# Kernel tuning notes

Hardware: AMD Instinct MI355X
Metric: run time of the kernel (lower is better)

The kernel has to match this reference:

```python
import jax, jax.numpy as jnp
import numpy as np

DIM = 768
NUM_HEADS = 12
HEAD_DIM = DIM // NUM_HEADS


def setup_inputs() -> dict:
    key = jax.random.key(0)
    k1, k2, k3 = jax.random.split(key, 3)
    B, N, C = 8, 4096, DIM
    x = jax.random.normal(k1, (B, N, C), dtype=jnp.float32)
    # torch nn.Linear weights are (out_features, in_features)
    W_qkv = jax.random.normal(k2, (3 * C, C), dtype=jnp.float32) * 0.02
    b_qkv = jnp.zeros((3 * C,), dtype=jnp.float32)
    W_proj = jax.random.normal(k3, (C, C), dtype=jnp.float32) * 0.02
    b_proj = jnp.zeros((C,), dtype=jnp.float32)
    return {"x": x, "W_qkv": W_qkv, "b_qkv": b_qkv, "W_proj": W_proj, "b_proj": b_proj}


def reference(x, W_qkv, b_qkv, W_proj, b_proj):
    B, N, C = x.shape
    H, D = NUM_HEADS, HEAD_DIM
    # qkv projection -> (3, B, H, N, D)
    qkv = (x @ W_qkv.T + b_qkv).reshape(B, N, 3, H, D).transpose(2, 0, 3, 1, 4)
    q, k, v = qkv[0], qkv[1], qkv[2]
    # feature map: elu(x) + 1 (positive kernel features)
    q = jax.nn.elu(q) + 1.0
    k = jax.nn.elu(k) + 1.0
    # kernelized linear attention: (K^T V) then Q (K^T V)
    kv = jnp.einsum('bhnd,bhnv->bhdv', k, v)          # (B,H,D,D)
    out = jnp.einsum('bhnd,bhdv->bhnv', q, kv)        # (B,H,N,D)
    k_sum = k.sum(axis=2)                             # (B,H,D)
    normalizer = jnp.einsum('bhnd,bhd->bhn', q, k_sum) + 1e-06
    out = out / normalizer[..., None]
    out = out.transpose(0, 2, 1, 3).reshape(B, N, C)
    out = out @ W_proj.T + b_proj
    return out
```

## Files before the change

kernel.cpp:

```cpp
#include <hip/hip_runtime.h>
#include <hip/hip_fp16.h>
#include <math.h>

#define NHEADS 12
#define SEQ 4096
#define BATCH 8

typedef _Float16 half8 __attribute__((ext_vector_type(8)));
typedef float floatx4 __attribute__((ext_vector_type(4)));

__global__ void zero_kernel(float* p, int n) {
  int i = blockIdx.x * 256 + threadIdx.x;
  if (i < n) p[i] = 0.f;
}

__global__ void cast_f2h(const float* __restrict__ in, __half* __restrict__ out, int n) {
  int i = (blockIdx.x * 256 + threadIdx.x) * 4;
  if (i < n) {
    float4 v = *(const float4*)&in[i];
    ushort4 o;
    o.x = __half_as_ushort(__float2half(v.x));
    o.y = __half_as_ushort(__float2half(v.y));
    o.z = __half_as_ushort(__float2half(v.z));
    o.w = __half_as_ushort(__float2half(v.w));
    *(ushort4*)&out[i] = o;
  }
}

__device__ __forceinline__ void stage_tile(const __half* __restrict__ gbase, int ldg,
                                           _Float16* lds, int t) {
#pragma unroll
  for (int it = 0; it < 2; ++it) {
    const int s  = it * 256 + t;
    const int mp = s >> 3, ps = s & 7;
    const int p  = ps ^ (mp & 7);
    const int r  = mp * 2 + (p >> 2);
    const int q  = p & 3;
    const __half* g = gbase + (size_t)r * ldg + q * 8;
    _Float16* dst = lds + (s >> 6) * 512;
    __builtin_amdgcn_global_load_lds((const __attribute__((address_space(1))) void*)g,
                                     (__attribute__((address_space(3))) void*)dst, 16, 0, 0);
  }
}
__device__ __forceinline__ half8 read_frag(const _Float16* lds, int row, int quad) {
  const int mp = row >> 1;
  const int p  = ((row & 1) << 2) | quad;
  const int ps = p ^ (mp & 7);
  return *(const half8*)(lds + (mp * 8 + ps) * 8);
}

__device__ __forceinline__ void write_l64(_Float16* lds, int row, int col, float v) {
  lds[row * 64 + ((((col >> 3) ^ (row & 7))) << 3) + (col & 7)] = (_Float16)v;
}
__device__ __forceinline__ half8 read_l64c(const _Float16* lds, int row, int c) {
  return *(const half8*)(lds + row * 64 + ((c ^ (row & 7)) << 3));
}

template<int MODE>
__global__ __launch_bounds__(256) void hgemm_kernel(
    const __half* __restrict__ A, const __half* __restrict__ W,
    const float* __restrict__ bias,
    __half* __restrict__ outK, __half* __restrict__ outV,
    float* __restrict__ outF, int colBase)
{
  const int K = 768;
  __shared__ __align__(16) _Float16 sh[16384];
  _Float16* As = sh;
  _Float16* Bs = sh + 4096;
  const int t    = threadIdx.x;
  const int w    = t >> 6;
  const int l    = t & 63;
  const int quad = l >> 4;
  const int mrow = l & 15;
  const int m0   = blockIdx.x * 128;
  const int j0   = blockIdx.y * 128;
  const int wr   = (w >> 1) * 64;
  const int wc   = (w & 1) * 64;

  floatx4 acc[4][4];
#pragma unroll
  for (int i = 0; i < 4; ++i)
#pragma unroll
    for (int j = 0; j < 4; ++j) acc[i][j] = (floatx4){0.f, 0.f, 0.f, 0.f};

  for (int k0 = 0; k0 < K; k0 += 32) {
    __syncthreads();
    stage_tile(A + (size_t)m0 * K + k0, K, As, t);
    stage_tile(W + (size_t)(colBase + j0) * K + k0, K, Bs, t);
    __syncthreads();
    half8 af[4], bf[4];
#pragma unroll
    for (int i = 0; i < 4; ++i) af[i] = read_frag(As, wr + i * 16 + mrow, quad);
#pragma unroll
    for (int j = 0; j < 4; ++j) bf[j] = read_frag(Bs, wc + j * 16 + mrow, quad);
#pragma unroll
    for (int i = 0; i < 4; ++i)
#pragma unroll
      for (int j = 0; j < 4; ++j)
        acc[i][j] = __builtin_amdgcn_mfma_f32_16x16x32_f16(af[i], bf[j], acc[i][j], 0, 0, 0);
  }

  if (MODE == 0) {
#pragma unroll
    for (int j = 0; j < 4; ++j) {
      const int col = colBase + j0 + wc + j * 16 + mrow;
      const float bsv = bias[col];
#pragma unroll
      for (int i = 0; i < 4; ++i)
#pragma unroll
        for (int r = 0; r < 4; ++r) {
          const int m = m0 + wr + i * 16 + quad * 4 + r;
          outF[(size_t)m * 768 + col] = acc[i][j][r] + bsv;
        }
    }
    return;
  }

  const int col0 = colBase + j0 + wc;
  const int t3   = col0 / 768;
  const int h    = (col0 - t3 * 768) >> 6;
  __half* dst    = (t3 == 1) ? outK : outV;
  const int m0w  = m0 + wr;
  const int b_   = m0w >> 12;
  const int n0w  = m0w & 4095;
  _Float16* scr  = sh + w * 4096;

  __syncthreads();
#pragma unroll
  for (int j = 0; j < 4; ++j) {
    const int col = j * 16 + mrow;
    const float bsv = bias[col0 + col];
#pragma unroll
    for (int i = 0; i < 4; ++i)
#pragma unroll
      for (int r = 0; r < 4; ++r) {
        const int row = i * 16 + quad * 4 + r;
        float val = acc[i][j][r] + bsv;
        if (t3 == 1) val = (val > 0.f) ? (val + 1.f) : expf(val);
        write_l64(scr, row, col, val);
      }
  }
  __syncthreads();
  const size_t gb = ((size_t)(b_ * NHEADS + h) * SEQ + n0w) * 64;
#pragma unroll
  for (int it = 0; it < 8; ++it) {
    const int row = it * 8 + (l >> 3);
    const int c   = l & 7;
    half8 vv = read_l64c(scr, row, c);
    *(half8*)((_Float16*)dst + gb + (size_t)row * 64 + c * 8) = vv;
  }
}

__global__ __launch_bounds__(256) void kv_kernel(
    const __half* __restrict__ k, const __half* __restrict__ v,
    float* __restrict__ kv, float* __restrict__ ksum)
{
  __shared__ float ks[32 * 64];
  __shared__ float vs[32 * 64];
  const int bh = blockIdx.x;
  const int s  = blockIdx.y;
  const int t  = threadIdx.x;
  const int w  = t >> 6;
  const int l  = t & 63;
  const size_t base = (size_t)bh * SEQ * 64 + (size_t)s * 512 * 64;

  float acc[16];
#pragma unroll
  for (int i = 0; i < 16; ++i) acc[i] = 0.f;
  float kspart = 0.f;

  const int nn0 = t >> 3;
  const int c8  = (t & 7) * 8;

  for (int chunk = 0; chunk < 512; chunk += 32) {
    __syncthreads();
    {
      half8 kk = *(const half8*)&k[base + (size_t)(chunk + nn0) * 64 + c8];
      half8 vv = *(const half8*)&v[base + (size_t)(chunk + nn0) * 64 + c8];
#pragma unroll
      for (int e = 0; e < 8; ++e) {
        ks[nn0 * 64 + c8 + e] = (float)kk[e];
        vs[nn0 * 64 + c8 + e] = (float)vv[e];
      }
    }
    __syncthreads();
#pragma unroll 4
    for (int nn = 0; nn < 32; ++nn) {
      const float ve = vs[nn * 64 + l];
      const float4* kr = (const float4*)&ks[nn * 64 + w * 16];
      float4 k0 = kr[0], k1 = kr[1], k2 = kr[2], k3 = kr[3];
      acc[0]  += k0.x * ve; acc[1]  += k0.y * ve; acc[2]  += k0.z * ve; acc[3]  += k0.w * ve;
      acc[4]  += k1.x * ve; acc[5]  += k1.y * ve; acc[6]  += k1.z * ve; acc[7]  += k1.w * ve;
      acc[8]  += k2.x * ve; acc[9]  += k2.y * ve; acc[10] += k2.z * ve; acc[11] += k2.w * ve;
      acc[12] += k3.x * ve; acc[13] += k3.y * ve; acc[14] += k3.z * ve; acc[15] += k3.w * ve;
      kspart += ks[nn * 64 + l];
    }
  }
#pragma unroll
  for (int i = 0; i < 16; ++i) {
    const int d = w * 16 + i;
    atomicAdd(&kv[((size_t)bh * 64 + d) * 64 + l], acc[i]);
  }
  if (t < 64) atomicAdd(&ksum[(size_t)bh * 64 + l], kspart);
}

__global__ __launch_bounds__(256) void qattn_kernel(
    const __half* __restrict__ A, const __half* __restrict__ W,
    const float* __restrict__ bias,
    const float* __restrict__ kvg, const float* __restrict__ ksumg,
    __half* __restrict__ att)
{
  const int K = 768;
  __shared__ __align__(16) _Float16 sh[24576];
  _Float16* As = sh;
  _Float16* Bs = sh + 4096;
  __shared__ float norms[256];
  __shared__ float ksums[128];
  const int t    = threadIdx.x;
  const int w    = t >> 6;
  const int l    = t & 63;
  const int quad = l >> 4;
  const int mrow = l & 15;
  const int m0   = blockIdx.x * 128;
  const int j0   = blockIdx.y * 128;
  const int wr   = (w >> 1) * 64;
  const int wc   = (w & 1) * 64;
  const int b_   = m0 >> 12;
  const int h0   = j0 >> 6;

  {
    _Float16* kvT0 = sh + 16384;
#pragma unroll
    for (int ii = 0; ii < 32; ++ii) {
      const int gidx = ii * 256 + t;
      const int head = gidx >> 12;
      const int r    = gidx & 4095;
      const float val = kvg[(size_t)(b_ * NHEADS + h0 + head) * 4096 + r];
      write_l64(kvT0 + head * 4096, r & 63, r >> 6, val);
    }
    if (t < 128) ksums[t] = ksumg[(size_t)(b_ * NHEADS + h0 + (t >> 6)) * 64 + (t & 63)];
  }

  floatx4 acc[4][4];
#pragma unroll
  for (int i = 0; i < 4; ++i)
#pragma unroll
    for (int j = 0; j < 4; ++j) acc[i][j] = (floatx4){0.f, 0.f, 0.f, 0.f};

  for (int k0 = 0; k0 < K; k0 += 32) {
    __syncthreads();
    stage_tile(A + (size_t)m0 * K + k0, K, As, t);
    stage_tile(W + (size_t)j0 * K + k0, K, Bs, t);
    __syncthreads();
    half8 af[4], bf[4];
#pragma unroll
    for (int i = 0; i < 4; ++i) af[i] = read_frag(As, wr + i * 16 + mrow, quad);
#pragma unroll
    for (int j = 0; j < 4; ++j) bf[j] = read_frag(Bs, wc + j * 16 + mrow, quad);
#pragma unroll
    for (int i = 0; i < 4; ++i)
#pragma unroll
      for (int j = 0; j < 4; ++j)
        acc[i][j] = __builtin_amdgcn_mfma_f32_16x16x32_f16(af[i], bf[j], acc[i][j], 0, 0, 0);
  }

  _Float16* qtile = sh + w * 4096;
  const _Float16* kvT = sh + 16384 + (w & 1) * 4096;
  const int hh = w & 1;

  __syncthreads();
#pragma unroll
  for (int j = 0; j < 4; ++j) {
    const int col = j * 16 + mrow;
    const float bsv = bias[j0 + wc + col];
#pragma unroll
    for (int i = 0; i < 4; ++i)
#pragma unroll
      for (int r = 0; r < 4; ++r) {
        const int row = i * 16 + quad * 4 + r;
        float val = acc[i][j][r] + bsv;
        val = (val > 0.f) ? (val + 1.f) : expf(val);
        write_l64(qtile, row, col, val);
      }
  }
  __syncthreads();

  {
    float nrm = 0.f;
#pragma unroll
    for (int c = 0; c < 8; ++c) {
      half8 qv = read_l64c(qtile, l, c);
#pragma unroll
      for (int e = 0; e < 8; ++e) nrm += (float)qv[e] * ksums[hh * 64 + c * 8 + e];
    }
    norms[w * 64 + l] = 1.f / (nrm + 1e-6f);
  }

  floatx4 oacc[4][4];
#pragma unroll
  for (int i = 0; i < 4; ++i)
#pragma unroll
    for (int j = 0; j < 4; ++j) oacc[i][j] = (floatx4){0.f, 0.f, 0.f, 0.f};
#pragma unroll
  for (int ks = 0; ks < 2; ++ks) {
    half8 af[4], bf[4];
#pragma unroll
    for (int i = 0; i < 4; ++i) af[i] = read_l64c(qtile, i * 16 + mrow, ks * 4 + quad);
#pragma unroll
    for (int j = 0; j < 4; ++j) bf[j] = read_l64c(kvT, j * 16 + mrow, ks * 4 + quad);
#pragma unroll
    for (int i = 0; i < 4; ++i)
#pragma unroll
      for (int j = 0; j < 4; ++j)
        oacc[i][j] = __builtin_amdgcn_mfma_f32_16x16x32_f16(af[i], bf[j], oacc[i][j], 0, 0, 0);
  }
  __syncthreads();

#pragma unroll
  for (int i = 0; i < 4; ++i)
#pragma unroll
    for (int r = 0; r < 4; ++r) {
      const int row = i * 16 + quad * 4 + r;
      const float rn = norms[w * 64 + row];
#pragma unroll
      for (int j = 0; j < 4; ++j)
        write_l64(qtile, row, j * 16 + mrow, oacc[i][j][r] * rn);
    }
  __syncthreads();
  const int n0w = (m0 & 4095) + wr;
  const size_t abase = (size_t)(b_ * SEQ + n0w) * 768 + (h0 + hh) * 64;
#pragma unroll
  for (int it = 0; it < 8; ++it) {
    const int row = it * 8 + (l >> 3);
    const int c   = l & 7;
    half8 vv = read_l64c(qtile, row, c);
    *(half8*)((_Float16*)att + abase + (size_t)row * 768 + c * 8) = vv;
  }
}

extern "C" void kernel_launch(void* const* d_in, const int* in_sizes, int n_in,
                              void* d_out, int out_size, void* d_ws, size_t ws_size,
                              hipStream_t stream)
{
  const float* x     = (const float*)d_in[0];
  const float* Wqkv  = (const float*)d_in[1];
  const float* bqkv  = (const float*)d_in[2];
  const float* Wproj = (const float*)d_in[3];
  const float* bproj = (const float*)d_in[4];
  float* out = (float*)d_out;

  const size_t SZ = (size_t)BATCH * NHEADS * SEQ * 64;
  __half* xh  = (__half*)d_ws;
  __half* Wqh = xh + SZ;
  __half* Wph = Wqh + (size_t)2304 * 768;
  __half* R3  = Wph + (size_t)768 * 768;
  __half* R4  = R3 + SZ;
  float*  kvb = (float*)(R4 + SZ);
  float*  ksum = kvb + 96 * 64 * 64;

  zero_kernel<<<1560, 256, 0, stream>>>(kvb, 96 * 64 * 64 + 96 * 64);

  cast_f2h<<<(int)(SZ / 1024), 256, 0, stream>>>(x, xh, (int)SZ);
  cast_f2h<<<(2304 * 768) / 1024, 256, 0, stream>>>(Wqkv, Wqh, 2304 * 768);
  cast_f2h<<<(768 * 768) / 1024, 256, 0, stream>>>(Wproj, Wph, 768 * 768);

  hgemm_kernel<1><<<dim3(256, 12), 256, 0, stream>>>(
      xh, Wqh, bqkv, R3, R4, nullptr, 768);

  kv_kernel<<<dim3(96, 8), 256, 0, stream>>>(R3, R4, kvb, ksum);

  qattn_kernel<<<dim3(256, 6), 256, 0, stream>>>(
      xh, Wqh, bqkv, kvb, ksum, R3);

  hgemm_kernel<0><<<dim3(256, 6), 256, 0, stream>>>(
      R3, Wph, bproj, nullptr, nullptr, out, 0);
}
```

Measured before the change: 505.4 us.

## Replace 128x128 HGEMM with 256x256 four-stage pipelined 512-thread GEMM

Swaps the 128x128 single-buffered GEMM for a 256x256 tile with 8 waves, a four-deep LDS ring buffer using async global-to-LDS loads, explicit vmcnt waits and raw barriers, and an XCD-aware block swizzle. The goal is to hide global load latency behind MFMA work and raise operand reuse per block. It also uses s_setprio around the MFMA bursts. The cost is 128KB of dynamic LDS per block and hand-counted waitcnt logic, which caps occupancy and is easy to get wrong.

```diff
diff --git a/kernel.cpp b/kernel.cpp
--- a/kernel.cpp
+++ b/kernel.cpp
@@ -42,6 +42,17 @@
                                      (__attribute__((address_space(3))) void*)dst, 16, 0, 0);
   }
 }
+__device__ __forceinline__ void stage_blk(const __half* __restrict__ gbase, int ldg,
+                                          _Float16* lds, int t) {
+  const int mp = t >> 3, ps = t & 7;
+  const int p  = ps ^ (mp & 7);
+  const int r  = mp * 2 + (p >> 2);
+  const int q  = p & 3;
+  const __half* g = gbase + (size_t)r * ldg + q * 8;
+  _Float16* dst = lds + (t >> 6) * 512;
+  __builtin_amdgcn_global_load_lds((const __attribute__((address_space(1))) void*)g,
+                                   (__attribute__((address_space(3))) void*)dst, 16, 0, 0);
+}
 __device__ __forceinline__ half8 read_frag(const _Float16* lds, int row, int quad) {
   const int mp = row >> 1;
   const int p  = ((row & 1) << 2) | quad;
@@ -56,98 +67,155 @@
   return *(const half8*)(lds + row * 64 + ((c ^ (row & 7)) << 3));
 }
 
+__device__ __forceinline__ void barrier_raw() {
+  asm volatile("s_barrier" ::: "memory");
+}
+
 template<int MODE>
-__global__ __launch_bounds__(256) void hgemm_kernel(
+__global__ __launch_bounds__(512, 2) void hgemm256_kernel(
     const __half* __restrict__ A, const __half* __restrict__ W,
     const float* __restrict__ bias,
     __half* __restrict__ outK, __half* __restrict__ outV,
     float* __restrict__ outF, int colBase)
 {
   const int K = 768;
-  __shared__ __align__(16) _Float16 sh[16384];
-  _Float16* As = sh;
-  _Float16* Bs = sh + 4096;
+  const int NT = 24;
+  extern __shared__ __align__(16) _Float16 sh[];
   const int t    = threadIdx.x;
   const int w    = t >> 6;
   const int l    = t & 63;
   const int quad = l >> 4;
   const int mrow = l & 15;
-  const int m0   = blockIdx.x * 128;
-  const int j0   = blockIdx.y * 128;
-  const int wr   = (w >> 1) * 64;
-  const int wc   = (w & 1) * 64;
-
-  floatx4 acc[4][4];
-#pragma unroll
-  for (int i = 0; i < 4; ++i)
+  const int wm   = w >> 2;
+  const int wn   = w & 3;
+
+  const int nwg  = gridDim.x;
+  const int cpx  = nwg >> 3;
+  const int bid  = blockIdx.x;
+  const int swz  = (bid & 7) * cpx + (bid >> 3);
+  const int m0   = (swz & 127) * 256;
+  const int j0   = (swz >> 7) * 256;
+
+  floatx4 acc[8][4];
+#pragma unroll
+  for (int i = 0; i < 8; ++i)
 #pragma unroll
     for (int j = 0; j < 4; ++j) acc[i][j] = (floatx4){0.f, 0.f, 0.f, 0.f};
 
-  for (int k0 = 0; k0 < K; k0 += 32) {
-    __syncthreads();
-    stage_tile(A + (size_t)m0 * K + k0, K, As, t);
-    stage_tile(W + (size_t)(colBase + j0) * K + k0, K, Bs, t);
-    __syncthreads();
+#pragma unroll
+  for (int kt = 0; kt < 3; ++kt) {
+    _Float16* db = sh + kt * 16384;
+    const int kg = kt * 32;
+    stage_blk(A + (size_t)m0 * K + kg, K, db, t);
+    stage_blk(A + (size_t)(m0 + 128) * K + kg, K, db + 4096, t);
+    stage_blk(W + (size_t)(colBase + j0) * K + kg, K, db + 8192, t);
+    stage_blk(W + (size_t)(colBase + j0 + 128) * K + kg, K, db + 12288, t);
+  }
+  asm volatile("s_waitcnt vmcnt(8)" ::: "memory");
+  barrier_raw();
+
+#pragma unroll 4
+  for (int kt = 0; kt < NT; ++kt) {
+    const _Float16* bb = sh + (kt & 3) * 16384;
+    const bool st = (kt + 3 < NT);
+    _Float16* db = sh + ((kt + 3) & 3) * 16384;
+    const int kg = (kt + 3) * 32;
     half8 af[4], bf[4];
-#pragma unroll
-    for (int i = 0; i < 4; ++i) af[i] = read_frag(As, wr + i * 16 + mrow, quad);
-#pragma unroll
-    for (int j = 0; j < 4; ++j) bf[j] = read_frag(Bs, wc + j * 16 + mrow, quad);
+
+#pragma unroll
+    for (int j = 0; j < 4; ++j) {
+      const int C = wn * 64 + j * 16 + mrow;
+      bf[j] = read_frag(bb + 8192 + (C >> 7) * 4096, C & 127, quad);
+    }
+#pragma unroll
+    for (int i = 0; i < 4; ++i)
+      af[i] = read_frag(bb + wm * 4096, i * 16 + mrow, quad);
+    if (st) {
+      stage_blk(A + (size_t)m0 * K + kg, K, db, t);
+      stage_blk(A + (size_t)(m0 + 128) * K + kg, K, db + 4096, t);
+    }
+    barrier_raw();
+    __builtin_amdgcn_s_setprio(1);
 #pragma unroll
     for (int i = 0; i < 4; ++i)
 #pragma unroll
       for (int j = 0; j < 4; ++j)
         acc[i][j] = __builtin_amdgcn_mfma_f32_16x16x32_f16(af[i], bf[j], acc[i][j], 0, 0, 0);
+    __builtin_amdgcn_s_setprio(0);
+
+#pragma unroll
+    for (int i = 0; i < 4; ++i)
+      af[i] = read_frag(bb + wm * 4096, (i + 4) * 16 + mrow, quad);
+    if (st) {
+      stage_blk(W + (size_t)(colBase + j0) * K + kg, K, db + 8192, t);
+      stage_blk(W + (size_t)(colBase + j0 + 128) * K + kg, K, db + 12288, t);
+    }
+    barrier_raw();
+    __builtin_amdgcn_s_setprio(1);
+#pragma unroll
+    for (int i = 0; i < 4; ++i)
+#pragma unroll
+      for (int j = 0; j < 4; ++j)
+        acc[i + 4][j] = __builtin_amdgcn_mfma_f32_16x16x32_f16(af[i], bf[j], acc[i + 4][j], 0, 0, 0);
+    __builtin_amdgcn_s_setprio(0);
+
+    if (kt < NT - 3)       asm volatile("s_waitcnt vmcnt(8)" ::: "memory");
+    else if (kt == NT - 3) asm volatile("s_waitcnt vmcnt(4)" ::: "memory");
+    else                   asm volatile("s_waitcnt vmcnt(0)" ::: "memory");
+    barrier_raw();
   }
 
   if (MODE == 0) {
 #pragma unroll
     for (int j = 0; j < 4; ++j) {
-      const int col = colBase + j0 + wc + j * 16 + mrow;
+      const int col = j0 + wn * 64 + j * 16 + mrow;
       const float bsv = bias[col];
 #pragma unroll
-      for (int i = 0; i < 4; ++i)
+      for (int i = 0; i < 8; ++i)
 #pragma unroll
         for (int r = 0; r < 4; ++r) {
-          const int m = m0 + wr + i * 16 + quad * 4 + r;
+          const int m = m0 + wm * 128 + i * 16 + quad * 4 + r;
           outF[(size_t)m * 768 + col] = acc[i][j][r] + bsv;
         }
     }
     return;
   }
 
-  const int col0 = colBase + j0 + wc;
+  const int col0 = colBase + j0 + wn * 64;
   const int t3   = col0 / 768;
   const int h    = (col0 - t3 * 768) >> 6;
   __half* dst    = (t3 == 1) ? outK : outV;
-  const int m0w  = m0 + wr;
+  const int m0w  = m0 + wm * 128;
   const int b_   = m0w >> 12;
   const int n0w  = m0w & 4095;
   _Float16* scr  = sh + w * 4096;
 
-  __syncthreads();
-#pragma unroll
-  for (int j = 0; j < 4; ++j) {
-    const int col = j * 16 + mrow;
-    const float bsv = bias[col0 + col];
-#pragma unroll
-    for (int i = 0; i < 4; ++i)
-#pragma unroll
-      for (int r = 0; r < 4; ++r) {
-        const int row = i * 16 + quad * 4 + r;
-        float val = acc[i][j][r] + bsv;
-        if (t3 == 1) val = (val > 0.f) ? (val + 1.f) : expf(val);
-        write_l64(scr, row, col, val);
-      }
-  }
-  __syncthreads();
-  const size_t gb = ((size_t)(b_ * NHEADS + h) * SEQ + n0w) * 64;
-#pragma unroll
-  for (int it = 0; it < 8; ++it) {
-    const int row = it * 8 + (l >> 3);
-    const int c   = l & 7;
-    half8 vv = read_l64c(scr, row, c);
-    *(half8*)((_Float16*)dst + gb + (size_t)row * 64 + c * 8) = vv;
+#pragma unroll
+  for (int hf = 0; hf < 2; ++hf) {
+#pragma unroll
+    for (int j = 0; j < 4; ++j) {
+      const int col = j * 16 + mrow;
+      const float bsv = bias[col0 + col];
+#pragma unroll
+      for (int ii = 0; ii < 4; ++ii)
+#pragma unroll
+        for (int r = 0; r < 4; ++r) {
+          const int row = ii * 16 + quad * 4 + r;
+          float val = acc[hf * 4 + ii][j][r] + bsv;
+          if (t3 == 1) val = (val > 0.f) ? (val + 1.f) : expf(val);
+          write_l64(scr, row, col, val);
+        }
+    }
+    barrier_raw();
+    const size_t gb = ((size_t)(b_ * NHEADS + h) * SEQ + n0w + hf * 64) * 64;
+#pragma unroll
+    for (int it = 0; it < 8; ++it) {
+      const int row = it * 8 + (l >> 3);
+      const int c   = l & 7;
+      half8 vv = read_l64c(scr, row, c);
+      *(half8*)((_Float16*)dst + gb + (size_t)row * 64 + c * 8) = vv;
+    }
+    barrier_raw();
   }
 }
 
@@ -358,13 +426,22 @@
   float*  kvb = (float*)(R4 + SZ);
   float*  ksum = kvb + 96 * 64 * 64;
 
+  static bool attr_set = false;
+  if (!attr_set) {
+    hipFuncSetAttribute((const void*)hgemm256_kernel<1>,
+                        hipFuncAttributeMaxDynamicSharedMemorySize, 131072);
+    hipFuncSetAttribute((const void*)hgemm256_kernel<0>,
+                        hipFuncAttributeMaxDynamicSharedMemorySize, 131072);
+    attr_set = true;
+  }
+
   zero_kernel<<<1560, 256, 0, stream>>>(kvb, 96 * 64 * 64 + 96 * 64);
 
   cast_f2h<<<(int)(SZ / 1024), 256, 0, stream>>>(x, xh, (int)SZ);
   cast_f2h<<<(2304 * 768) / 1024, 256, 0, stream>>>(Wqkv, Wqh, 2304 * 768);
   cast_f2h<<<(768 * 768) / 1024, 256, 0, stream>>>(Wproj, Wph, 768 * 768);
 
-  hgemm_kernel<1><<<dim3(256, 12), 256, 0, stream>>>(
+  hgemm256_kernel<1><<<768, 512, 131072, stream>>>(
       xh, Wqh, bqkv, R3, R4, nullptr, 768);
 
   kv_kernel<<<dim3(96, 8), 256, 0, stream>>>(R3, R4, kvb, ksum);
@@ -372,6 +449,6 @@
   qattn_kernel<<<dim3(256, 6), 256, 0, stream>>>(
       xh, Wqh, bqkv, kvb, ksum, R3);
 
-  hgemm_kernel<0><<<dim3(256, 6), 256, 0, stream>>>(
+  hgemm256_kernel<0><<<384, 512, 131072, stream>>>(
       R3, Wph, bproj, nullptr, nullptr, out, 0);
 }
```

Measured after the change: 524.7 us. 3.8% more time.

## Add dedicated 128x256-tile K/V projection GEMM with XCD-aware block mapping

Applied to the files above, without the earlier changes.

Replaces the generic hgemm_kernel for the K/V projection with a new kernel that uses 512-thread blocks, 128x256 output tiles, double-buffered LDS staging through global_load_lds, and a block-index remap so that consecutive M tiles stay on the same XCD. The epilogue adds the bias, applies the elu+1 feature map to K, and writes through LDS scratch to get coalesced half8 stores. The intent is more operand reuse per tile, overlap of loads with MFMA work, and better L2 locality. In exchange it needs 48KB of dynamic LDS and higher register pressure, which may limit occupancy.

```diff
diff --git a/kernel.cpp b/kernel.cpp
--- a/kernel.cpp
+++ b/kernel.cpp
@@ -42,6 +42,17 @@
                                      (__attribute__((address_space(3))) void*)dst, 16, 0, 0);
   }
 }
+__device__ __forceinline__ void stage_blk(const __half* __restrict__ gbase, int ldg,
+                                          _Float16* lds, int t) {
+  const int mp = t >> 3, ps = t & 7;
+  const int p  = ps ^ (mp & 7);
+  const int r  = mp * 2 + (p >> 2);
+  const int q  = p & 3;
+  const __half* g = gbase + (size_t)r * ldg + q * 8;
+  _Float16* dst = lds + (t >> 6) * 512;
+  __builtin_amdgcn_global_load_lds((const __attribute__((address_space(1))) void*)g,
+                                   (__attribute__((address_space(3))) void*)dst, 16, 0, 0);
+}
 __device__ __forceinline__ half8 read_frag(const _Float16* lds, int row, int quad) {
   const int mp = row >> 1;
   const int p  = ((row & 1) << 2) | quad;
@@ -54,6 +65,120 @@
 }
 __device__ __forceinline__ half8 read_l64c(const _Float16* lds, int row, int c) {
   return *(const half8*)(lds + row * 64 + ((c ^ (row & 7)) << 3));
+}
+
+__device__ __forceinline__ void barrier_raw() {
+  asm volatile("s_barrier" ::: "memory");
+}
+
+__global__ __launch_bounds__(512, 4) void hgemm_kv_kernel(
+    const __half* __restrict__ A, const __half* __restrict__ W,
+    const float* __restrict__ bias,
+    __half* __restrict__ outK, __half* __restrict__ outV)
+{
+  const int K = 768;
+  const int NT = 24;
+  extern __shared__ __align__(16) _Float16 sh[];
+  const int t    = threadIdx.x;
+  const int w    = t >> 6;
+  const int l    = t & 63;
+  const int quad = l >> 4;
+  const int mrow = l & 15;
+  const int wm   = w >> 2;
+  const int wn   = w & 3;
+
+  const int bid  = blockIdx.x;
+  const int xcd  = bid & 7;
+  const int ii   = bid >> 3;
+  const int mg   = ii / 6;
+  const int jj   = ii - mg * 6;
+  const int m0   = (xcd * 32 + mg) * 128;
+  const int j0   = jj * 256;
+
+  floatx4 acc[4][4];
+#pragma unroll
+  for (int i = 0; i < 4; ++i)
+#pragma unroll
+    for (int j = 0; j < 4; ++j) acc[i][j] = (floatx4){0.f, 0.f, 0.f, 0.f};
+
+  stage_blk(A + (size_t)m0 * K, K, sh, t);
+  stage_blk(W + (size_t)(768 + j0) * K, K, sh + 4096, t);
+  stage_blk(W + (size_t)(768 + j0 + 128) * K, K, sh + 8192, t);
+  asm volatile("s_waitcnt vmcnt(0)" ::: "memory");
+  barrier_raw();
+
+#pragma unroll 2
+  for (int kt = 0; kt < NT; ++kt) {
+    const _Float16* bb = sh + (kt & 1) * 12288;
+    _Float16* db = sh + ((kt + 1) & 1) * 12288;
+    const bool st = (kt + 1 < NT);
+    const int kg = (kt + 1) * 32;
+
+    if (st) {
+      stage_blk(A + (size_t)m0 * K + kg, K, db, t);
+      stage_blk(W + (size_t)(768 + j0) * K + kg, K, db + 4096, t);
+      stage_blk(W + (size_t)(768 + j0 + 128) * K + kg, K, db + 8192, t);
+    }
+
+    half8 af[4], bf[4];
+#pragma unroll
+    for (int j = 0; j < 4; ++j) {
+      const int C = wn * 64 + j * 16 + mrow;
+      bf[j] = read_frag(bb + 4096 + (C >> 7) * 4096, C & 127, quad);
+    }
+#pragma unroll
+    for (int i = 0; i < 4; ++i)
+      af[i] = read_frag(bb, wm * 64 + i * 16 + mrow, quad);
+#pragma unroll
+    for (int i = 0; i < 4; ++i)
+#pragma unroll
+      for (int j = 0; j < 4; ++j)
+        acc[i][j] = __builtin_amdgcn_mfma_f32_16x16x32_f16(af[i], bf[j], acc[i][j], 0, 0, 0);
+
+    if (st) asm volatile("s_waitcnt vmcnt(0)" ::: "memory");
+    barrier_raw();
+  }
+
+  const int col0 = 768 + j0 + wn * 64;
+  const int t3   = col0 / 768;
+  const int h    = (col0 - t3 * 768) >> 6;
+  __half* dst    = (t3 == 1) ? outK : outV;
+  const int m0w  = m0 + wm * 64;
+  const int b_   = m0w >> 12;
+  const int n0w  = m0w & 4095;
+  _Float16* scr  = sh + wn * 4096;
+  const size_t gb = ((size_t)(b_ * NHEADS + h) * SEQ + n0w) * 64;
+
+#pragma unroll
+  for (int p = 0; p < 2; ++p) {
+    if (wm == p) {
+#pragma unroll
+      for (int j = 0; j < 4; ++j) {
+        const int col = j * 16 + mrow;
+        const float bsv = bias[col0 + col];
+#pragma unroll
+        for (int i = 0; i < 4; ++i)
+#pragma unroll
+          for (int r = 0; r < 4; ++r) {
+            const int row = i * 16 + quad * 4 + r;
+            float val = acc[i][j][r] + bsv;
+            if (t3 == 1) val = (val > 0.f) ? (val + 1.f) : expf(val);
+            write_l64(scr, row, col, val);
+          }
+      }
+    }
+    barrier_raw();
+    if (wm == p) {
+#pragma unroll
+      for (int it = 0; it < 8; ++it) {
+        const int row = it * 8 + (l >> 3);
+        const int c   = l & 7;
+        half8 vv = read_l64c(scr, row, c);
+        *(half8*)((_Float16*)dst + gb + (size_t)row * 64 + c * 8) = vv;
+      }
+    }
+    barrier_raw();
+  }
 }
 
 template<int MODE>
@@ -364,8 +489,7 @@
   cast_f2h<<<(2304 * 768) / 1024, 256, 0, stream>>>(Wqkv, Wqh, 2304 * 768);
   cast_f2h<<<(768 * 768) / 1024, 256, 0, stream>>>(Wproj, Wph, 768 * 768);
 
-  hgemm_kernel<1><<<dim3(256, 12), 256, 0, stream>>>(
-      xh, Wqh, bqkv, R3, R4, nullptr, 768);
+  hgemm_kv_kernel<<<1536, 512, 49152, stream>>>(xh, Wqh, bqkv, R3, R4);
 
   kv_kernel<<<dim3(96, 8), 256, 0, stream>>>(R3, R4, kvb, ksum);
 
```

New measurement: 516.4 us. 1.02x slower.
